# Performance work log

Measured on AMD Instinct MI355X. Metric: run time of the kernel, lower is better.

## Reference

```python
import jax, jax.numpy as jnp
import numpy as np

# --- static config (from init_kwargs) ---
B = 256        # num graphs
NPG = 128      # nodes per graph
EPG = 512      # edges per graph
DIN = 128      # dim_node
D = 256        # dim_hidden
RATIO = 0.5    # causal_ratio
N_RES = int(RATIO * EPG)
BN_EPS = 1e-5


def setup_inputs() -> dict:
    key = jax.random.key(0)
    ks = jax.random.split(key, 24)
    N = B * NPG
    x = jax.random.normal(ks[0], (N, DIN), jnp.float32)
    # edges confined within each graph, contiguous per graph (graph-sorted)
    src = jax.random.randint(ks[1], (B, EPG), 0, NPG)
    dst = jax.random.randint(ks[2], (B, EPG), 0, NPG)
    off = (jnp.arange(B, dtype=jnp.int32) * NPG)[:, None]
    edge_index = jnp.stack([(src + off).reshape(-1), (dst + off).reshape(-1)], 0).astype(jnp.int32)
    batch = jnp.repeat(jnp.arange(B, dtype=jnp.int32), NPG)

    s = 0.05
    def rn(k, shape):
        return jax.random.normal(k, shape, jnp.float32) * s
    p = dict(
        x=x, edge_index=edge_index, batch=batch,
        vemb=rn(ks[3], (1, D)),
        # conv1 GIN mlp: Linear(DIN,2D) -> BN -> ReLU -> Linear(2D,D)
        W1a=rn(ks[4], (DIN, 2 * D)), b1a=jnp.zeros((2 * D,)),
        g1a=jnp.ones((2 * D,)), be1a=jnp.zeros((2 * D,)),
        W1b=rn(ks[5], (2 * D, D)), b1b=jnp.zeros((D,)),
        g1=jnp.ones((D,)), be1=jnp.zeros((D,)),          # outer batch_norm1
        # conv2 GIN mlp
        W2a=rn(ks[6], (D, 2 * D)), b2a=jnp.zeros((2 * D,)),
        g2a=jnp.ones((2 * D,)), be2a=jnp.zeros((2 * D,)),
        W2b=rn(ks[7], (2 * D, D)), b2b=jnp.zeros((D,)),
        g2=jnp.ones((D,)), be2=jnp.zeros((D,)),          # outer batch_norm2
        # edge scorer: Linear(2D, 1)
        Wl=rn(ks[8], (2 * D, 1)), bl=jnp.zeros((1,)),
    )
    return p


def _bn(h, g, b):
    mu = h.mean(0)
    var = jnp.mean((h - mu) ** 2, 0)
    return (h - mu) * jax.lax.rsqrt(var + BN_EPS) * g + b


def reference(x, edge_index, batch, vemb,
              W1a, b1a, g1a, be1a, W1b, b1b, g1, be1,
              W2a, b2a, g2a, be2a, W2b, b2b, g2, be2,
              Wl, bl):
    N = x.shape[0]
    row, col = edge_index[0], edge_index[1]

    def gin(h, Wa, ba, ga, bta, Wb, bb):
        # GINConv, eps=0: mlp(h + sum_{j->i} h_j), aggregate src feats at dst
        agg = jax.ops.segment_sum(h[row], col, num_segments=N)
        z = (h + agg) @ Wa + ba
        z = jax.nn.relu(_bn(z, ga, bta))
        return z @ Wb + bb

    # layer 1: conv1 -> bn -> relu (dropout_rate = 0)
    post = jax.nn.relu(_bn(gin(x, W1a, b1a, g1a, be1a, W1b, b1b), g1, be1))
    # virtual node gather (embedding of index 0, one per graph)
    vfeat = jnp.broadcast_to(vemb[0], (B, D))
    post = post + vfeat[batch]
    # layer 2 (last): conv2 -> bn, no relu
    xn = _bn(gin(post, W2a, b2a, g2a, be2a, W2b, b2b), g2, be2)

    # edge scoring
    erep = jnp.concatenate([xn[row], xn[col]], axis=-1)          # [E, 2D]
    pred = (erep @ Wl + bl.astype(erep.dtype)).reshape(-1)       # [E]

    # per-graph top-k split (equal EPG edges per graph)
    pw = pred.reshape(B, EPG)
    order = jnp.argsort(-pw, axis=1)
    idx_r, idx_d = order[:, :N_RES], order[:, N_RES:]
    causal_w = jnp.take_along_axis(pw, idx_r, 1).reshape(-1)
    conf_w = -jnp.take_along_axis(pw, idx_d, 1).reshape(-1)
    ei = edge_index.reshape(2, B, EPG)
    causal_ei = jnp.take_along_axis(ei, jnp.broadcast_to(idx_r[None], (2, B, N_RES)), axis=2).reshape(2, -1)
    conf_ei = jnp.take_along_axis(ei, jnp.broadcast_to(idx_d[None], (2, B, EPG - N_RES)), axis=2).reshape(2, -1)
    return (causal_ei, causal_w, conf_ei, conf_w, pred)
```

## Files before the change

kernel.cpp:

```cpp
#include <hip/hip_runtime.h>

#define BGR   256
#define NPG   128
#define EPG   512
#define DIN   128
#define DD    256
#define DD2   512
#define NTOT  (BGR * NPG)
#define ETOT  (BGR * EPG)
#define NRES  (EPG / 2)
#define NCHUNK 256
#define MP    136

#define OFF_CEI  0
#define OFF_CW   (2 * BGR * NRES)
#define OFF_FEI  (OFF_CW + BGR * NRES)
#define OFF_FW   (OFF_FEI + 2 * BGR * NRES)
#define OFF_PRED (OFF_FW + BGR * NRES)

typedef unsigned short ushortt;
typedef __attribute__((ext_vector_type(4))) unsigned short us4;
typedef __attribute__((ext_vector_type(8))) unsigned short us8;
typedef __attribute__((ext_vector_type(8))) short short8;
typedef __attribute__((ext_vector_type(4))) float f32x4;

__device__ __forceinline__ ushortt f2bf(float f) {
    unsigned int u = __float_as_uint(f);
    unsigned int r = (u + 0x7fffu + ((u >> 16) & 1u)) >> 16;
    return (ushortt)r;
}
__device__ __forceinline__ float bf2f(ushortt u) {
    return __uint_as_float(((unsigned int)u) << 16);
}

__device__ __forceinline__ void g2lds16(const void* g, void* l) {
    __builtin_amdgcn_global_load_lds(
        (const __attribute__((address_space(1))) unsigned int*)g,
        (__attribute__((address_space(3))) unsigned int*)l, 16, 0, 0);
}

__global__ __launch_bounds__(256) void prep(const float* __restrict__ W1a,
                                            const float* __restrict__ W1b,
                                            const float* __restrict__ W2a,
                                            const float* __restrict__ W2b,
                                            const float* __restrict__ x,
                                            const int* __restrict__ ei,
                                            ushortt* __restrict__ Wt1a,
                                            ushortt* __restrict__ Wt1b,
                                            ushortt* __restrict__ Wt2a,
                                            ushortt* __restrict__ Wt2b,
                                            ushortt* __restrict__ Madj,
                                            ushortt* __restrict__ s1) {
    __shared__ __align__(16) char smem[102400];
    const int t = threadIdx.x;
    if (blockIdx.x < 1792) {
        const int idx = blockIdx.x * 256 + t;
        if (idx < 65536) {
            const int k = idx >> 9, n = idx & 511;
            Wt1a[n * DIN + k] = f2bf(W1a[idx]);
        } else if (idx < 196608) {
            const int i = idx - 65536;
            const int k = i >> 8, n = i & 255;
            Wt1b[n * DD2 + k] = f2bf(W1b[i]);
        } else if (idx < 327680) {
            const int i = idx - 196608;
            const int k = i >> 9, n = i & 511;
            Wt2a[n * DD + k] = f2bf(W2a[i]);
        } else if (idx < 458752) {
            const int i = idx - 327680;
            const int k = i >> 8, n = i & 255;
            Wt2b[n * DD2 + k] = f2bf(W2b[i]);
        }
        return;
    }
    const int b = blockIdx.x - 1792;
    ushortt* Ms = (ushortt*)smem;
    int* cnt = (int*)(smem + 34816);
    ushortt* XT = (ushortt*)(smem + 34816);
    ushortt* Cs = (ushortt*)(smem + 69632);
    const int wave = t >> 6, lane = t & 63;
    const int qd = lane >> 4, r = lane & 15;
    const int wm = (wave >> 1) * 64, wn = (wave & 1) * 64;

    for (int i = t; i < NPG * NPG; i += 256) cnt[i] = 0;
    __syncthreads();
    for (int e = t; e < EPG; e += 256) {
        const int src = ei[b * EPG + e] - b * NPG;
        const int dst = ei[ETOT + b * EPG + e] - b * NPG;
        atomicAdd(&cnt[dst * NPG + src], 1);
    }
    __syncthreads();
#pragma unroll
    for (int k = 0; k < 8; ++k) {
        const int ch = t + k * 256;
        const int m = ch >> 4, sc = (ch & 15) * 8;
        us8 o;
#pragma unroll
        for (int e = 0; e < 8; ++e)
            o[e] = f2bf((float)(cnt[m * NPG + sc + e] + (m == sc + e ? 1 : 0)));
        *(us8*)&Ms[m * MP + sc] = o;
        *(us8*)&Madj[(size_t)b * NPG * NPG + m * NPG + sc] = o;
    }
    __syncthreads();

#pragma unroll
    for (int k = 0; k < 8; ++k) {
        const int ch = t + k * 256;
        const int c = ch & 127, s8 = ch >> 7;
        us8 o;
#pragma unroll
        for (int j = 0; j < 8; ++j)
            o[j] = f2bf(x[(size_t)(b * NPG + s8 * 8 + j) * DIN + c]);
        *(us8*)&XT[c * MP + s8 * 8] = o;
    }
    __syncthreads();

    f32x4 acc[4][4] = {};
#pragma unroll
    for (int ks = 0; ks < 4; ++ks) {
        const int k0 = ks * 32 + qd * 8;
        short8 af[4], bfr[4];
#pragma unroll
        for (int i = 0; i < 4; ++i)
            af[i] = *(const short8*)&Ms[(wm + i * 16 + r) * MP + k0];
#pragma unroll
        for (int j = 0; j < 4; ++j)
            bfr[j] = *(const short8*)&XT[(wn + j * 16 + r) * MP + k0];
#pragma unroll
        for (int i = 0; i < 4; ++i)
#pragma unroll
            for (int j = 0; j < 4; ++j)
                acc[i][j] = __builtin_amdgcn_mfma_f32_16x16x32_bf16(af[i], bfr[j], acc[i][j], 0, 0, 0);
    }
#pragma unroll
    for (int j = 0; j < 4; ++j) {
        const int coll = wn + j * 16 + r;
#pragma unroll
        for (int i = 0; i < 4; ++i)
#pragma unroll
            for (int tt = 0; tt < 4; ++tt)
                Cs[(wm + i * 16 + qd * 4 + tt) * 128 + coll] = f2bf(acc[i][j][tt]);
    }
    __syncthreads();
#pragma unroll
    for (int k = 0; k < 8; ++k) {
        const int ch = t + k * 256;
        const int row = ch >> 4, colc = (ch & 15) * 8;
        *(us8*)&s1[(size_t)(b * NPG + row) * DIN + colc] = *(const us8*)&Cs[row * 128 + colc];
    }
}

#define BM 128
#define BN 128
#define BK 32
__global__ __launch_bounds__(256) void gemm_mfma(const ushortt* __restrict__ A,
                                                 const ushortt* __restrict__ Wt,
                                                 const float* __restrict__ bias,
                                                 ushortt* __restrict__ C,
                                                 float* __restrict__ psum,
                                                 float* __restrict__ psumsq,
                                                 int M, int N, int K) {
    __shared__ ushortt As[BM * BK];
    __shared__ ushortt Bs[BN * BK];
    __shared__ ushortt Cs[BM * BN];
    __shared__ float redS[2][BN];
    __shared__ float redQ[2][BN];
    const int tid  = threadIdx.x;
    const int wave = tid >> 6;
    const int lane = tid & 63;
    const int qd = lane >> 4;
    const int r  = lane & 15;
    const int wm = (wave >> 1) * 64;
    const int wn = (wave & 1) * 64;
    const int m0 = blockIdx.y * BM;
    const int n0 = blockIdx.x * BN;

    f32x4 acc[4][4] = {};

    for (int k0 = 0; k0 < K; k0 += BK) {
#pragma unroll
        for (int s = 0; s < 2; ++s) {
            const int o   = wave * 128 + s * 64 + lane;
            const int row = o >> 2;
            const int cg  = o & 3;
            g2lds16(A  + (size_t)(m0 + row) * K + k0 + cg * 8,
                    &As[(size_t)(wave * 128 + s * 64) * 8]);
            g2lds16(Wt + (size_t)(n0 + row) * K + k0 + cg * 8,
                    &Bs[(size_t)(wave * 128 + s * 64) * 8]);
        }
        __syncthreads();
        short8 af[4], bfr[4];
#pragma unroll
        for (int i = 0; i < 4; ++i)
            af[i] = *(const short8*)&As[(wm + i * 16 + r) * BK + qd * 8];
#pragma unroll
        for (int j = 0; j < 4; ++j)
            bfr[j] = *(const short8*)&Bs[(wn + j * 16 + r) * BK + qd * 8];
#pragma unroll
        for (int i = 0; i < 4; ++i)
#pragma unroll
            for (int j = 0; j < 4; ++j)
                acc[i][j] = __builtin_amdgcn_mfma_f32_16x16x32_bf16(af[i], bfr[j], acc[i][j], 0, 0, 0);
        __syncthreads();
    }

#pragma unroll
    for (int j = 0; j < 4; ++j) {
        const int coll = wn + j * 16 + r;
        const float bv = bias[n0 + coll];
        float s = 0.0f, q = 0.0f;
#pragma unroll
        for (int i = 0; i < 4; ++i)
#pragma unroll
            for (int t = 0; t < 4; ++t) {
                const float v = acc[i][j][t] + bv;
                Cs[(wm + i * 16 + qd * 4 + t) * BN + coll] = f2bf(v);
                s += v;
                q = fmaf(v, v, q);
            }
        s += __shfl_xor(s, 16); s += __shfl_xor(s, 32);
        q += __shfl_xor(q, 16); q += __shfl_xor(q, 32);
        if (qd == 0) {
            redS[wave >> 1][coll] = s;
            redQ[wave >> 1][coll] = q;
        }
    }
    __syncthreads();
    if (tid < BN) {
        psum[(size_t)blockIdx.y * N + n0 + tid]   = redS[0][tid] + redS[1][tid];
        psumsq[(size_t)blockIdx.y * N + n0 + tid] = redQ[0][tid] + redQ[1][tid];
    }
#pragma unroll
    for (int s8 = 0; s8 < 8; ++s8) {
        const int c    = tid + 256 * s8;
        const int row  = c >> 4;
        const int colc = (c & 15) * 8;
        const us8 v = *(const us8*)&Cs[row * BN + colc];
        *(us8*)&C[(size_t)(m0 + row) * N + n0 + colc] = v;
    }
}

__global__ __launch_bounds__(256) void bn_finalize(const float* __restrict__ psum,
                                                   const float* __restrict__ psumsq,
                                                   const float* __restrict__ g,
                                                   const float* __restrict__ be,
                                                   int ncols,
                                                   float* __restrict__ scale,
                                                   float* __restrict__ shift) {
    const int c = blockIdx.x * 256 + threadIdx.x;
    double s = 0.0, s2 = 0.0;
    for (int k = 0; k < NCHUNK; ++k) {
        s += (double)psum[(size_t)k * ncols + c];
        s2 += (double)psumsq[(size_t)k * ncols + c];
    }
    const double mean = s / (double)NTOT;
    const double var = s2 / (double)NTOT - mean * mean;
    const double rs = 1.0 / sqrt(var + 1e-5);
    const float sc = (float)((double)g[c] * rs);
    scale[c] = sc;
    shift[c] = (float)((double)be[c] - mean * (double)sc);
}

__global__ __launch_bounds__(256) void gemm_bn(const ushortt* __restrict__ A,
                                               const ushortt* __restrict__ Wt,
                                               const float* __restrict__ scale,
                                               const float* __restrict__ shift,
                                               const float* __restrict__ bias,
                                               ushortt* __restrict__ C,
                                               float* __restrict__ psOut,
                                               float* __restrict__ pqOut) {
    __shared__ ushortt As[BM * BK];
    __shared__ ushortt Bs[BN * BK];
    __shared__ ushortt Cs[BM * BN];
    __shared__ float redS[2][BN];
    __shared__ float redQ[2][BN];
    __shared__ float scs[DD2], shs[DD2];
    const int tid  = threadIdx.x;
    const int wave = tid >> 6;
    const int lane = tid & 63;
    const int qd = lane >> 4;
    const int r  = lane & 15;
    const int wm = (wave >> 1) * 64;
    const int wn = (wave & 1) * 64;
    const int m0 = blockIdx.y * BM;
    const int n0 = blockIdx.x * BN;
    const int K = DD2, N = DD;

    for (int i = tid; i < K; i += 256) {
        scs[i] = scale[i];
        shs[i] = shift[i];
    }
    __syncthreads();

    f32x4 acc[4][4] = {};

    for (int k0 = 0; k0 < K; k0 += BK) {
#pragma unroll
        for (int s = 0; s < 2; ++s) {
            const int o   = wave * 128 + s * 64 + lane;
            const int row = o >> 2;
            const int cg  = o & 3;
            g2lds16(Wt + (size_t)(n0 + row) * K + k0 + cg * 8,
                    &Bs[(size_t)(wave * 128 + s * 64) * 8]);
        }
#pragma unroll
        for (int s = 0; s < 2; ++s) {
            const int o   = wave * 128 + s * 64 + lane;
            const int row = o >> 2;
            const int cg  = o & 3;
            const us8 a8 = *(const us8*)&A[(size_t)(m0 + row) * K + k0 + cg * 8];
            const float4 s4a = *(const float4*)&scs[k0 + cg * 8];
            const float4 s4b = *(const float4*)&scs[k0 + cg * 8 + 4];
            const float4 h4a = *(const float4*)&shs[k0 + cg * 8];
            const float4 h4b = *(const float4*)&shs[k0 + cg * 8 + 4];
            us8 t8;
            t8[0] = f2bf(fmaxf(fmaf(bf2f(a8[0]), s4a.x, h4a.x), 0.0f));
            t8[1] = f2bf(fmaxf(fmaf(bf2f(a8[1]), s4a.y, h4a.y), 0.0f));
            t8[2] = f2bf(fmaxf(fmaf(bf2f(a8[2]), s4a.z, h4a.z), 0.0f));
            t8[3] = f2bf(fmaxf(fmaf(bf2f(a8[3]), s4a.w, h4a.w), 0.0f));
            t8[4] = f2bf(fmaxf(fmaf(bf2f(a8[4]), s4b.x, h4b.x), 0.0f));
            t8[5] = f2bf(fmaxf(fmaf(bf2f(a8[5]), s4b.y, h4b.y), 0.0f));
            t8[6] = f2bf(fmaxf(fmaf(bf2f(a8[6]), s4b.z, h4b.z), 0.0f));
            t8[7] = f2bf(fmaxf(fmaf(bf2f(a8[7]), s4b.w, h4b.w), 0.0f));
            *(us8*)&As[row * BK + cg * 8] = t8;
        }
        __syncthreads();
        short8 af[4], bfr[4];
#pragma unroll
        for (int i = 0; i < 4; ++i)
            af[i] = *(const short8*)&As[(wm + i * 16 + r) * BK + qd * 8];
#pragma unroll
        for (int j = 0; j < 4; ++j)
            bfr[j] = *(const short8*)&Bs[(wn + j * 16 + r) * BK + qd * 8];
#pragma unroll
        for (int i = 0; i < 4; ++i)
#pragma unroll
            for (int j = 0; j < 4; ++j)
                acc[i][j] = __builtin_amdgcn_mfma_f32_16x16x32_bf16(af[i], bfr[j], acc[i][j], 0, 0, 0);
        __syncthreads();
    }

#pragma unroll
    for (int j = 0; j < 4; ++j) {
        const int coll = wn + j * 16 + r;
        const float bv = bias[n0 + coll];
        float s = 0.0f, q = 0.0f;
#pragma unroll
        for (int i = 0; i < 4; ++i)
#pragma unroll
            for (int t = 0; t < 4; ++t) {
                const float v = acc[i][j][t] + bv;
                Cs[(wm + i * 16 + qd * 4 + t) * BN + coll] = f2bf(v);
                s += v;
                q = fmaf(v, v, q);
            }
        s += __shfl_xor(s, 16); s += __shfl_xor(s, 32);
        q += __shfl_xor(q, 16); q += __shfl_xor(q, 32);
        if (qd == 0) {
            redS[wave >> 1][coll] = s;
            redQ[wave >> 1][coll] = q;
        }
    }
    __syncthreads();
    if (tid < BN) {
        psOut[(size_t)blockIdx.y * N + n0 + tid] = redS[0][tid] + redS[1][tid];
        pqOut[(size_t)blockIdx.y * N + n0 + tid] = redQ[0][tid] + redQ[1][tid];
    }
#pragma unroll
    for (int s8 = 0; s8 < 8; ++s8) {
        const int c    = tid + 256 * s8;
        const int row  = c >> 4;
        const int colc = (c & 15) * 8;
        const us8 v = *(const us8*)&Cs[row * BN + colc];
        *(us8*)&C[(size_t)(m0 + row) * N + n0 + colc] = v;
    }
}

__global__ __launch_bounds__(256) void agg2_mm(const ushortt* __restrict__ h,
                                               const float* __restrict__ psum,
                                               const float* __restrict__ psumsq,
                                               const float* __restrict__ g,
                                               const float* __restrict__ be,
                                               const float* __restrict__ vemb,
                                               const ushortt* __restrict__ Madj,
                                               ushortt* __restrict__ s2) {
    __shared__ ushortt Ms[NPG * MP];
    __shared__ ushortt PT[NPG * MP];
    __shared__ double redS[2][128];
    __shared__ double redQ[2][128];
    __shared__ float scs[128], shs[128];
    const int nb = blockIdx.x, b = blockIdx.y, t = threadIdx.x;
    const int wave = t >> 6, lane = t & 63;
    const int qd = lane >> 4, r = lane & 15;
    const int wm = (wave >> 1) * 64, wn = (wave & 1) * 64;
    const ushortt* Mg = Madj + (size_t)b * NPG * NPG;
#pragma unroll
    for (int k = 0; k < 8; ++k) {
        const int ch = t + k * 256;
        const int m = ch >> 4, sc = (ch & 15) * 8;
        *(us8*)&Ms[m * MP + sc] = *(const us8*)&Mg[m * NPG + sc];
    }
    {
        const int cl = t & 127, half = t >> 7;
        const int c = nb * 128 + cl;
        double s = 0.0, q = 0.0;
#pragma unroll 4
        for (int k = half * 128; k < half * 128 + 128; ++k) {
            s += (double)psum[(size_t)k * DD + c];
            q += (double)psumsq[(size_t)k * DD + c];
        }
        redS[half][cl] = s;
        redQ[half][cl] = q;
    }
    __syncthreads();
    if (t < 128) {
        const int c = nb * 128 + t;
        const double s = redS[0][t] + redS[1][t];
        const double q = redQ[0][t] + redQ[1][t];
        const double mean = s / (double)NTOT;
        const double var = q / (double)NTOT - mean * mean;
        const double rs = 1.0 / sqrt(var + 1e-5);
        const float sc = (float)((double)g[c] * rs);
        scs[t] = sc;
        shs[t] = (float)((double)be[c] - mean * (double)sc);
    }
    __syncthreads();
#pragma unroll
    for (int k = 0; k < 8; ++k) {
        const int ch = t + k * 256;
        const int cl = ch & 127, s8 = ch >> 7;
        const float scv = scs[cl], shv = shs[cl], vev = vemb[nb * 128 + cl];
        us8 o;
#pragma unroll
        for (int j = 0; j < 8; ++j) {
            float v = fmaf(bf2f(h[(size_t)(b * NPG + s8 * 8 + j) * DD + nb * 128 + cl]), scv, shv);
            o[j] = f2bf(fmaxf(v, 0.0f) + vev);
        }
        *(us8*)&PT[cl * MP + s8 * 8] = o;
    }
    __syncthreads();
    f32x4 acc[4][4] = {};
#pragma unroll
    for (int ks = 0; ks < 4; ++ks) {
        const int k0 = ks * 32 + qd * 8;
        short8 af[4], bfr[4];
#pragma unroll
        for (int i = 0; i < 4; ++i)
            af[i] = *(const short8*)&Ms[(wm + i * 16 + r) * MP + k0];
#pragma unroll
        for (int j = 0; j < 4; ++j)
            bfr[j] = *(const short8*)&PT[(wn + j * 16 + r) * MP + k0];
#pragma unroll
        for (int i = 0; i < 4; ++i)
#pragma unroll
            for (int j = 0; j < 4; ++j)
                acc[i][j] = __builtin_amdgcn_mfma_f32_16x16x32_bf16(af[i], bfr[j], acc[i][j], 0, 0, 0);
    }
    __syncthreads();
    ushortt* Cs = Ms;
#pragma unroll
    for (int j = 0; j < 4; ++j) {
        const int coll = wn + j * 16 + r;
#pragma unroll
        for (int i = 0; i < 4; ++i)
#pragma unroll
            for (int tt = 0; tt < 4; ++tt)
                Cs[(wm + i * 16 + qd * 4 + tt) * 128 + coll] = f2bf(acc[i][j][tt]);
    }
    __syncthreads();
#pragma unroll
    for (int k = 0; k < 8; ++k) {
        const int ch = t + k * 256;
        const int row = ch >> 4, colc = (ch & 15) * 8;
        *(us8*)&s2[(size_t)(b * NPG + row) * DD + nb * 128 + colc] =
            *(const us8*)&Cs[row * 128 + colc];
    }
}

__global__ __launch_bounds__(EPG) void sort_mega(const ushortt* __restrict__ h2,
                                                 const float* __restrict__ psum,
                                                 const float* __restrict__ psumsq,
                                                 const float* __restrict__ g,
                                                 const float* __restrict__ be,
                                                 const float* __restrict__ Wl,
                                                 const float* __restrict__ bl,
                                                 const int* __restrict__ ei,
                                                 float* __restrict__ out) {
    __shared__ double redS[2][DD];
    __shared__ double redQ[2][DD];
    __shared__ float scs[DD], shs[DD];
    __shared__ float pa[NPG], pb[NPG];
    __shared__ float pw[EPG];
    __shared__ int ord[EPG];
    const int b = blockIdx.x, t = threadIdx.x;
    {
        const int c = t & 255, half = t >> 8;
        double s = 0.0, q = 0.0;
#pragma unroll 4
        for (int k = half * 128; k < half * 128 + 128; ++k) {
            s += (double)psum[(size_t)k * DD + c];
            q += (double)psumsq[(size_t)k * DD + c];
        }
        redS[half][c] = s;
        redQ[half][c] = q;
    }
    __syncthreads();
    if (t < DD) {
        const double s = redS[0][t] + redS[1][t];
        const double q = redQ[0][t] + redQ[1][t];
        const double mean = s / (double)NTOT;
        const double var = q / (double)NTOT - mean * mean;
        const double rs = 1.0 / sqrt(var + 1e-5);
        const float sc = (float)((double)g[t] * rs);
        scs[t] = sc;
        shs[t] = (float)((double)be[t] - mean * (double)sc);
    }
    __syncthreads();
    {
        const int wave = t >> 6, lane = t & 63;
        const float4 w0 = *(const float4*)&Wl[lane * 4];
        const float4 w1 = *(const float4*)&Wl[DD + lane * 4];
        const float4 sc4 = *(const float4*)&scs[lane * 4];
        const float4 sh4 = *(const float4*)&shs[lane * 4];
        for (int n = wave; n < NPG; n += 8) {
            const us4 z4 = *(const us4*)&h2[(size_t)(b * NPG + n) * DD + lane * 4];
            const float x0 = fmaf(bf2f(z4.x), sc4.x, sh4.x);
            const float x1 = fmaf(bf2f(z4.y), sc4.y, sh4.y);
            const float x2 = fmaf(bf2f(z4.z), sc4.z, sh4.z);
            const float x3 = fmaf(bf2f(z4.w), sc4.w, sh4.w);
            float sa = x0 * w0.x + x1 * w0.y + x2 * w0.z + x3 * w0.w;
            float sb = x0 * w1.x + x1 * w1.y + x2 * w1.z + x3 * w1.w;
#pragma unroll
            for (int off = 32; off >= 1; off >>= 1) {
                sa += __shfl_down(sa, off);
                sb += __shfl_down(sb, off);
            }
            if (lane == 0) { pa[n] = sa; pb[n] = sb; }
        }
    }
    __syncthreads();
    const int rl = ei[b * EPG + t] - b * NPG;
    const int cl = ei[ETOT + b * EPG + t] - b * NPG;
    const float v = pa[rl] + pb[cl] + bl[0];
    pw[t] = v;
    out[OFF_PRED + b * EPG + t] = v;
    __syncthreads();
    int rank = 0;
#pragma unroll 8
    for (int k = 0; k < EPG; ++k) {
        const float u = pw[k];
        rank += (u > v) || (u == v && k < t);
    }
    ord[rank] = t;
    __syncthreads();
    const int j = ord[t];
    const float wv = pw[j];
    const float e0 = (float)ei[b * EPG + j];
    const float e1 = (float)ei[ETOT + b * EPG + j];
    if (t < NRES) {
        out[OFF_CEI + b * NRES + t] = e0;
        out[OFF_CEI + BGR * NRES + b * NRES + t] = e1;
        out[OFF_CW + b * NRES + t] = wv;
    } else {
        const int p = t - NRES;
        out[OFF_FEI + b * NRES + p] = e0;
        out[OFF_FEI + BGR * NRES + b * NRES + p] = e1;
        out[OFF_FW + b * NRES + p] = -wv;
    }
}

extern "C" void kernel_launch(void* const* d_in, const int* in_sizes, int n_in,
                              void* d_out, int out_size, void* d_ws, size_t ws_size,
                              hipStream_t stream) {
    (void)in_sizes; (void)n_in; (void)out_size; (void)ws_size;
    const float* x    = (const float*)d_in[0];
    const int*   ei   = (const int*)d_in[1];
    const float* vemb = (const float*)d_in[3];
    const float* W1a  = (const float*)d_in[4];
    const float* b1a  = (const float*)d_in[5];
    const float* g1a  = (const float*)d_in[6];
    const float* be1a = (const float*)d_in[7];
    const float* W1b  = (const float*)d_in[8];
    const float* b1b  = (const float*)d_in[9];
    const float* g1   = (const float*)d_in[10];
    const float* be1  = (const float*)d_in[11];
    const float* W2a  = (const float*)d_in[12];
    const float* b2a  = (const float*)d_in[13];
    const float* g2a  = (const float*)d_in[14];
    const float* be2a = (const float*)d_in[15];
    const float* W2b  = (const float*)d_in[16];
    const float* b2b  = (const float*)d_in[17];
    const float* g2   = (const float*)d_in[18];
    const float* be2  = (const float*)d_in[19];
    const float* Wl   = (const float*)d_in[20];
    const float* bl   = (const float*)d_in[21];
    float* out = (float*)d_out;

    char* wp = (char*)d_ws;
    auto alloc = [&](size_t bytes) -> char* {
        char* r = wp;
        wp += (bytes + 255) & ~(size_t)255;
        return r;
    };
    ushortt* zb    = (ushortt*)alloc((size_t)NTOT * 512 * 2);
    ushortt* bufC  = (ushortt*)alloc((size_t)NTOT * 256 * 2);
    ushortt* bufS1 = (ushortt*)alloc((size_t)NTOT * 128 * 2);
    ushortt* bufS2 = (ushortt*)alloc((size_t)NTOT * 256 * 2);
    ushortt* Madj  = (ushortt*)alloc((size_t)BGR * NPG * NPG * 2);
    ushortt* Wt1a  = (ushortt*)alloc((size_t)DIN * DD2 * 2);
    ushortt* Wt1b  = (ushortt*)alloc((size_t)DD2 * DD * 2);
    ushortt* Wt2a  = (ushortt*)alloc((size_t)DD * DD2 * 2);
    ushortt* Wt2b  = (ushortt*)alloc((size_t)DD2 * DD * 2);
    float*   psA   = (float*)alloc((size_t)256 * DD2 * 4);
    float*   pqA   = (float*)alloc((size_t)256 * DD2 * 4);
    float*   psB   = (float*)alloc((size_t)256 * DD * 4);
    float*   pqB   = (float*)alloc((size_t)256 * DD * 4);
    float*   scA   = (float*)alloc(DD2 * 4);
    float*   shA   = (float*)alloc(DD2 * 4);

    prep<<<2048, 256, 0, stream>>>(W1a, W1b, W2a, W2b, x, ei,
                                   Wt1a, Wt1b, Wt2a, Wt2b, Madj, bufS1);

    gemm_mfma<<<dim3(DD2 / BN, NTOT / BM), 256, 0, stream>>>(bufS1, Wt1a, b1a, zb, psA, pqA, NTOT, DD2, DIN);
    bn_finalize<<<2, 256, 0, stream>>>(psA, pqA, g1a, be1a, DD2, scA, shA);

    gemm_bn<<<dim3(DD / BN, NTOT / BM), 256, 0, stream>>>(zb, Wt1b, scA, shA, b1b, bufC, psB, pqB);

    agg2_mm<<<dim3(2, BGR), 256, 0, stream>>>(bufC, psB, pqB, g1, be1, vemb, Madj, bufS2);

    gemm_mfma<<<dim3(DD2 / BN, NTOT / BM), 256, 0, stream>>>(bufS2, Wt2a, b2a, zb, psA, pqA, NTOT, DD2, DD);
    bn_finalize<<<2, 256, 0, stream>>>(psA, pqA, g2a, be2a, DD2, scA, shA);

    gemm_bn<<<dim3(DD / BN, NTOT / BM), 256, 0, stream>>>(zb, Wt2b, scA, shA, b2b, bufC, psB, pqB);

    sort_mega<<<BGR, EPG, 0, stream>>>(bufC, psB, pqB, g2, be2, Wl, bl, ei, out);
}
```

Measured before the change: 306.9 us.

## Fuse BN finalize into GEMM via last-block counter, tile weight transpose, shrink LDS

```diff
diff --git a/kernel.cpp b/kernel.cpp
--- a/kernel.cpp
+++ b/kernel.cpp
@@ -11,6 +11,7 @@
 #define NRES  (EPG / 2)
 #define NCHUNK 256
 #define MP    136
+#define CSP   72
 
 #define OFF_CEI  0
 #define OFF_CW   (2 * BGR * NRES)
@@ -50,30 +51,46 @@
                                             ushortt* __restrict__ Wt2a,
                                             ushortt* __restrict__ Wt2b,
                                             ushortt* __restrict__ Madj,
-                                            ushortt* __restrict__ s1) {
+                                            ushortt* __restrict__ s1,
+                                            int* __restrict__ counters) {
     __shared__ __align__(16) char smem[102400];
     const int t = threadIdx.x;
-    if (blockIdx.x < 1792) {
-        const int idx = blockIdx.x * 256 + t;
-        if (idx < 65536) {
-            const int k = idx >> 9, n = idx & 511;
-            Wt1a[n * DIN + k] = f2bf(W1a[idx]);
-        } else if (idx < 196608) {
-            const int i = idx - 65536;
-            const int k = i >> 8, n = i & 255;
-            Wt1b[n * DD2 + k] = f2bf(W1b[i]);
-        } else if (idx < 327680) {
-            const int i = idx - 196608;
-            const int k = i >> 9, n = i & 511;
-            Wt2a[n * DD + k] = f2bf(W2a[i]);
-        } else if (idx < 458752) {
-            const int i = idx - 327680;
-            const int k = i >> 8, n = i & 255;
-            Wt2b[n * DD2 + k] = f2bf(W2b[i]);
+    const int blk = blockIdx.x;
+    if (blk < 112) {
+        if (blk == 0 && t < 2) counters[t] = 0;
+        const float* W; ushortt* Wt; int Nsrc, Ktot, kr0, nc0;
+        if (blk < 16)       { W = W1a; Wt = Wt1a; Nsrc = 512; Ktot = 128;
+                              kr0 = (blk >> 3) * 64;        nc0 = (blk & 7) * 64; }
+        else if (blk < 48)  { const int i = blk - 16; W = W1b; Wt = Wt1b; Nsrc = 256; Ktot = 512;
+                              kr0 = (i >> 2) * 64;          nc0 = (i & 3) * 64; }
+        else if (blk < 80)  { const int i = blk - 48; W = W2a; Wt = Wt2a; Nsrc = 512; Ktot = 256;
+                              kr0 = (i >> 3) * 64;          nc0 = (i & 7) * 64; }
+        else                { const int i = blk - 80; W = W2b; Wt = Wt2b; Nsrc = 256; Ktot = 512;
+                              kr0 = (i >> 2) * 64;          nc0 = (i & 3) * 64; }
+        ushortt* tile = (ushortt*)smem;
+#pragma unroll
+        for (int kk = 0; kk < 4; ++kk) {
+            const int idx = t + kk * 256;
+            const int rr = idx >> 4, c4 = (idx & 15) * 4;
+            const float4 v = *(const float4*)&W[(size_t)(kr0 + rr) * Nsrc + nc0 + c4];
+            tile[rr * 67 + c4 + 0] = f2bf(v.x);
+            tile[rr * 67 + c4 + 1] = f2bf(v.y);
+            tile[rr * 67 + c4 + 2] = f2bf(v.z);
+            tile[rr * 67 + c4 + 3] = f2bf(v.w);
+        }
+        __syncthreads();
+#pragma unroll
+        for (int kk = 0; kk < 2; ++kk) {
+            const int idx = t + kk * 256;
+            const int n = idx >> 3, k8 = (idx & 7) * 8;
+            us8 o;
+#pragma unroll
+            for (int j = 0; j < 8; ++j) o[j] = tile[(k8 + j) * 67 + n];
+            *(us8*)&Wt[(size_t)(nc0 + n) * Ktot + kr0 + k8] = o;
         }
         return;
     }
-    const int b = blockIdx.x - 1792;
+    const int b = blk - 112;
     ushortt* Ms = (ushortt*)smem;
     int* cnt = (int*)(smem + 34816);
     ushortt* XT = (ushortt*)(smem + 34816);
@@ -153,18 +170,24 @@
 #define BM 128
 #define BN 128
 #define BK 32
-__global__ __launch_bounds__(256) void gemm_mfma(const ushortt* __restrict__ A,
-                                                 const ushortt* __restrict__ Wt,
-                                                 const float* __restrict__ bias,
-                                                 ushortt* __restrict__ C,
-                                                 float* __restrict__ psum,
-                                                 float* __restrict__ psumsq,
-                                                 int M, int N, int K) {
-    __shared__ ushortt As[BM * BK];
-    __shared__ ushortt Bs[BN * BK];
-    __shared__ ushortt Cs[BM * BN];
+__global__ __launch_bounds__(256) void gemm_zf(const ushortt* __restrict__ A,
+                                               const ushortt* __restrict__ Wt,
+                                               const float* __restrict__ bias,
+                                               ushortt* __restrict__ C,
+                                               float* __restrict__ psum,
+                                               float* __restrict__ psumsq,
+                                               const float* __restrict__ g,
+                                               const float* __restrict__ be,
+                                               float* __restrict__ scale,
+                                               float* __restrict__ shift,
+                                               int* __restrict__ counter,
+                                               int M, int N, int K) {
+    __shared__ __align__(16) ushortt uni[BM * CSP];
     __shared__ float redS[2][BN];
     __shared__ float redQ[2][BN];
+    __shared__ int lastFlag;
+    ushortt* As = uni;
+    ushortt* Bs = uni + BM * BK;
     const int tid  = threadIdx.x;
     const int wave = tid >> 6;
     const int lane = tid & 63;
@@ -204,61 +227,70 @@
         __syncthreads();
     }
 
-#pragma unroll
-    for (int j = 0; j < 4; ++j) {
-        const int coll = wn + j * 16 + r;
-        const float bv = bias[n0 + coll];
-        float s = 0.0f, q = 0.0f;
-#pragma unroll
-        for (int i = 0; i < 4; ++i)
-#pragma unroll
-            for (int t = 0; t < 4; ++t) {
-                const float v = acc[i][j][t] + bv;
-                Cs[(wm + i * 16 + qd * 4 + t) * BN + coll] = f2bf(v);
-                s += v;
-                q = fmaf(v, v, q);
+    ushortt* Cs = uni;
+#pragma unroll
+    for (int p = 0; p < 2; ++p) {
+        if ((wn >> 6) == p) {
+#pragma unroll
+            for (int j = 0; j < 4; ++j) {
+                const int coll = wn + j * 16 + r;
+                const int cloc = coll & 63;
+                const float bv = bias[n0 + coll];
+                float s = 0.0f, q = 0.0f;
+#pragma unroll
+                for (int i = 0; i < 4; ++i)
+#pragma unroll
+                    for (int tt = 0; tt < 4; ++tt) {
+                        const float v = acc[i][j][tt] + bv;
+                        Cs[(wm + i * 16 + qd * 4 + tt) * CSP + cloc] = f2bf(v);
+                        s += v;
+                        q = fmaf(v, v, q);
+                    }
+                s += __shfl_xor(s, 16); s += __shfl_xor(s, 32);
+                q += __shfl_xor(q, 16); q += __shfl_xor(q, 32);
+                if (qd == 0) {
+                    redS[wave >> 1][coll] = s;
+                    redQ[wave >> 1][coll] = q;
+                }
             }
-        s += __shfl_xor(s, 16); s += __shfl_xor(s, 32);
-        q += __shfl_xor(q, 16); q += __shfl_xor(q, 32);
-        if (qd == 0) {
-            redS[wave >> 1][coll] = s;
-            redQ[wave >> 1][coll] = q;
-        }
-    }
-    __syncthreads();
+        }
+        __syncthreads();
+#pragma unroll
+        for (int s8 = 0; s8 < 4; ++s8) {
+            const int ch = tid + 256 * s8;
+            const int row = ch >> 3, colc = (ch & 7) * 8;
+            *(us8*)&C[(size_t)(m0 + row) * N + n0 + p * 64 + colc] =
+                *(const us8*)&Cs[row * CSP + colc];
+        }
+        __syncthreads();
+    }
     if (tid < BN) {
         psum[(size_t)blockIdx.y * N + n0 + tid]   = redS[0][tid] + redS[1][tid];
         psumsq[(size_t)blockIdx.y * N + n0 + tid] = redQ[0][tid] + redQ[1][tid];
     }
-#pragma unroll
-    for (int s8 = 0; s8 < 8; ++s8) {
-        const int c    = tid + 256 * s8;
-        const int row  = c >> 4;
-        const int colc = (c & 15) * 8;
-        const us8 v = *(const us8*)&Cs[row * BN + colc];
-        *(us8*)&C[(size_t)(m0 + row) * N + n0 + colc] = v;
-    }
-}
-
-__global__ __launch_bounds__(256) void bn_finalize(const float* __restrict__ psum,
-                                                   const float* __restrict__ psumsq,
-                                                   const float* __restrict__ g,
-                                                   const float* __restrict__ be,
-                                                   int ncols,
-                                                   float* __restrict__ scale,
-                                                   float* __restrict__ shift) {
-    const int c = blockIdx.x * 256 + threadIdx.x;
-    double s = 0.0, s2 = 0.0;
-    for (int k = 0; k < NCHUNK; ++k) {
-        s += (double)psum[(size_t)k * ncols + c];
-        s2 += (double)psumsq[(size_t)k * ncols + c];
-    }
-    const double mean = s / (double)NTOT;
-    const double var = s2 / (double)NTOT - mean * mean;
-    const double rs = 1.0 / sqrt(var + 1e-5);
-    const float sc = (float)((double)g[c] * rs);
-    scale[c] = sc;
-    shift[c] = (float)((double)be[c] - mean * (double)sc);
+    __threadfence();
+    __syncthreads();
+    if (tid == 0)
+        lastFlag = (atomicAdd(counter, 1) == (int)(gridDim.x * gridDim.y) - 1);
+    __syncthreads();
+    if (lastFlag) {
+        __threadfence();
+#pragma unroll
+        for (int h = 0; h < 2; ++h) {
+            const int c = tid + h * 256;
+            double s = 0.0, s2 = 0.0;
+            for (int k = 0; k < NCHUNK; ++k) {
+                s += (double)psum[(size_t)k * N + c];
+                s2 += (double)psumsq[(size_t)k * N + c];
+            }
+            const double mean = s / (double)NTOT;
+            const double var = s2 / (double)NTOT - mean * mean;
+            const double rs = 1.0 / sqrt(var + 1e-5);
+            const float sc = (float)((double)g[c] * rs);
+            scale[c] = sc;
+            shift[c] = (float)((double)be[c] - mean * (double)sc);
+        }
+    }
 }
 
 __global__ __launch_bounds__(256) void gemm_bn(const ushortt* __restrict__ A,
@@ -269,12 +301,12 @@
                                                ushortt* __restrict__ C,
                                                float* __restrict__ psOut,
                                                float* __restrict__ pqOut) {
-    __shared__ ushortt As[BM * BK];
-    __shared__ ushortt Bs[BN * BK];
-    __shared__ ushortt Cs[BM * BN];
+    __shared__ __align__(16) ushortt uni[BM * CSP];
     __shared__ float redS[2][BN];
     __shared__ float redQ[2][BN];
     __shared__ float scs[DD2], shs[DD2];
+    ushortt* As = uni;
+    ushortt* Bs = uni + BM * BK;
     const int tid  = threadIdx.x;
     const int wave = tid >> 6;
     const int lane = tid & 63;
@@ -340,39 +372,46 @@
         __syncthreads();
     }
 
-#pragma unroll
-    for (int j = 0; j < 4; ++j) {
-        const int coll = wn + j * 16 + r;
-        const float bv = bias[n0 + coll];
-        float s = 0.0f, q = 0.0f;
-#pragma unroll
-        for (int i = 0; i < 4; ++i)
-#pragma unroll
-            for (int t = 0; t < 4; ++t) {
-                const float v = acc[i][j][t] + bv;
-                Cs[(wm + i * 16 + qd * 4 + t) * BN + coll] = f2bf(v);
-                s += v;
-                q = fmaf(v, v, q);
+    ushortt* Cs = uni;
+#pragma unroll
+    for (int p = 0; p < 2; ++p) {
+        if ((wn >> 6) == p) {
+#pragma unroll
+            for (int j = 0; j < 4; ++j) {
+                const int coll = wn + j * 16 + r;
+                const int cloc = coll & 63;
+                const float bv = bias[n0 + coll];
+                float s = 0.0f, q = 0.0f;
+#pragma unroll
+                for (int i = 0; i < 4; ++i)
+#pragma unroll
+                    for (int tt = 0; tt < 4; ++tt) {
+                        const float v = acc[i][j][tt] + bv;
+                        Cs[(wm + i * 16 + qd * 4 + tt) * CSP + cloc] = f2bf(v);
+                        s += v;
+                        q = fmaf(v, v, q);
+                    }
+                s += __shfl_xor(s, 16); s += __shfl_xor(s, 32);
+                q += __shfl_xor(q, 16); q += __shfl_xor(q, 32);
+                if (qd == 0) {
+                    redS[wave >> 1][coll] = s;
+                    redQ[wave >> 1][coll] = q;
+                }
             }
-        s += __shfl_xor(s, 16); s += __shfl_xor(s, 32);
-        q += __shfl_xor(q, 16); q += __shfl_xor(q, 32);
-        if (qd == 0) {
-            redS[wave >> 1][coll] = s;
-            redQ[wave >> 1][coll] = q;
-        }
-    }
-    __syncthreads();
+        }
+        __syncthreads();
+#pragma unroll
+        for (int s8 = 0; s8 < 4; ++s8) {
+            const int ch = tid + 256 * s8;
+            const int row = ch >> 3, colc = (ch & 7) * 8;
+            *(us8*)&C[(size_t)(m0 + row) * N + n0 + p * 64 + colc] =
+                *(const us8*)&Cs[row * CSP + colc];
+        }
+        __syncthreads();
+    }
     if (tid < BN) {
         psOut[(size_t)blockIdx.y * N + n0 + tid] = redS[0][tid] + redS[1][tid];
         pqOut[(size_t)blockIdx.y * N + n0 + tid] = redQ[0][tid] + redQ[1][tid];
-    }
-#pragma unroll
-    for (int s8 = 0; s8 < 8; ++s8) {
-        const int c    = tid + 256 * s8;
-        const int row  = c >> 4;
-        const int colc = (c & 15) * 8;
-        const us8 v = *(const us8*)&Cs[row * BN + colc];
-        *(us8*)&C[(size_t)(m0 + row) * N + n0 + colc] = v;
     }
 }
 
@@ -617,19 +656,22 @@
     float*   pqB   = (float*)alloc((size_t)256 * DD * 4);
     float*   scA   = (float*)alloc(DD2 * 4);
     float*   shA   = (float*)alloc(DD2 * 4);
-
-    prep<<<2048, 256, 0, stream>>>(W1a, W1b, W2a, W2b, x, ei,
-                                   Wt1a, Wt1b, Wt2a, Wt2b, Madj, bufS1);
-
-    gemm_mfma<<<dim3(DD2 / BN, NTOT / BM), 256, 0, stream>>>(bufS1, Wt1a, b1a, zb, psA, pqA, NTOT, DD2, DIN);
-    bn_finalize<<<2, 256, 0, stream>>>(psA, pqA, g1a, be1a, DD2, scA, shA);
+    int*     cnts  = (int*)alloc(2 * 4);
+
+    prep<<<368, 256, 0, stream>>>(W1a, W1b, W2a, W2b, x, ei,
+                                  Wt1a, Wt1b, Wt2a, Wt2b, Madj, bufS1, cnts);
+
+    gemm_zf<<<dim3(DD2 / BN, NTOT / BM), 256, 0, stream>>>(bufS1, Wt1a, b1a, zb, psA, pqA,
+                                                           g1a, be1a, scA, shA, cnts + 0,
+                                                           NTOT, DD2, DIN);
 
     gemm_bn<<<dim3(DD / BN, NTOT / BM), 256, 0, stream>>>(zb, Wt1b, scA, shA, b1b, bufC, psB, pqB);
 
     agg2_mm<<<dim3(2, BGR), 256, 0, stream>>>(bufC, psB, pqB, g1, be1, vemb, Madj, bufS2);
 
-    gemm_mfma<<<dim3(DD2 / BN, NTOT / BM), 256, 0, stream>>>(bufS2, Wt2a, b2a, zb, psA, pqA, NTOT, DD2, DD);
-    bn_finalize<<<2, 256, 0, stream>>>(psA, pqA, g2a, be2a, DD2, scA, shA);
+    gemm_zf<<<dim3(DD2 / BN, NTOT / BM), 256, 0, stream>>>(bufS2, Wt2a, b2a, zb, psA, pqA,
+                                                           g2a, be2a, scA, shA, cnts + 1,
+                                                           NTOT, DD2, DD);
 
     gemm_bn<<<dim3(DD / BN, NTOT / BM), 256, 0, stream>>>(zb, Wt2b, scA, shA, b2b, bufC, psB, pqB);
 
```

New measurement: 564.1 us. 1.84x slower.
